# Kernel tuning notes

Measured on AMD Instinct MI355X. Metric: run time of the kernel, lower is better.

Reference implementation:

```python
import jax, jax.numpy as jnp
import numpy as np

VOCAB = 100000
EMB_DIM = 128
MAX_KP = 50  # config.max_num_keyphrases; lens tensors are constant-filled with this
EPS = 1e-8   # torch cosine_similarity eps


def setup_inputs() -> dict:
    key = jax.random.key(0)
    k1, k2, k3, k4 = jax.random.split(key, 4)
    B, A, K = 64, 32, 50
    batch_source = jax.random.randint(k1, (B, A, K), 0, VOCAB)
    pos_result = jax.random.randint(k2, (B, A, K), 0, VOCAB)
    neg_result = jax.random.randint(k3, (B, A, K), 0, VOCAB)
    emb_table = jax.random.normal(k4, (VOCAB + 1, EMB_DIM), dtype=jnp.float32)
    emb_table = emb_table.at[0].set(0.0)  # padding_idx=0
    return {
        "batch_source": batch_source,
        "pos_result": pos_result,
        "neg_result": neg_result,
        "emb_table": emb_table,
    }


def _embed(emb_table, idx):
    # idx: [B, A, K] -> mean-pooled [B, A, D]; denominator is the constant MAX_KP
    emb = emb_table[idx]                      # [B, A, K, D] gather (memory-bound)
    return jnp.sum(emb, axis=-2) / MAX_KP     # [B, A, D]


def _l2norm(x):
    n = jnp.sqrt(jnp.sum(x * x, axis=-1, keepdims=True))
    return x / jnp.maximum(n, EPS)


def _max_cosine(src_e, tgt_e):
    # src_e: [B, A1, D], tgt_e: [B, A2, D] -> max over all (A1, A2) pairs, per batch
    sims = jnp.einsum("bad,bcd->bac", _l2norm(src_e), _l2norm(tgt_e))  # [B, A1, A2]
    return jnp.max(sims, axis=(1, 2))  # [B]


def reference(batch_source, pos_result, neg_result, emb_table):
    src_e = _embed(emb_table, batch_source)
    pos_e = _embed(emb_table, pos_result)
    neg_e = _embed(emb_table, neg_result)
    pos_scores = _max_cosine(src_e, pos_e)  # [B]
    neg_scores = _max_cosine(src_e, neg_e)  # [B]
    x = pos_scores - neg_scores
    # BCEWithLogitsLoss with target = 1: mean(softplus(-x))
    loss = jnp.mean(jax.nn.softplus(-x))
    return loss
```

## Files before the change

kernel.cpp:

```cpp
#include <hip/hip_runtime.h>
#include <math.h>

#define BB 64
#define AA 32
#define KK 50
#define DD 128
#define MAX_KP 50
#define EPS_CS 1e-8f

__global__ void embed_norm_kernel(const int* __restrict__ src,
                                  const int* __restrict__ pos,
                                  const int* __restrict__ neg,
                                  const float* __restrict__ table,
                                  float* __restrict__ out )
{
    const int vec = blockIdx.x;
    const int t  = vec >> 11;
    const int ba = vec & 2047;

    const int* idx_base = (t == 0) ? src : (t == 1) ? pos : neg;
    idx_base += ba * KK;

    const int d = threadIdx.x;
    float acc = 0.f;
    #pragma unroll
    for (int k = 0; k < KK; ++k) {
        const int row = idx_base[k];
        acc += table[(long)row * DD + d];
    }
    acc *= (1.0f / MAX_KP);

    float sq = acc * acc;
    #pragma unroll
    for (int off = 32; off > 0; off >>= 1) sq += __shfl_down(sq, off, 64);

    __shared__ float partial[2];
    const int wave = threadIdx.x >> 6;
    if ((threadIdx.x & 63) == 0) partial[wave] = sq;
    __syncthreads();
    const float n2 = partial[0] + partial[1];
    const float nrm = sqrtf(n2);
    const float inv = 1.0f / fmaxf(nrm, EPS_CS);

    out[(long)vec * DD + d] = acc * inv;
}

__global__ void cosine_loss_kernel(const float* __restrict__ embs,
                                   float* __restrict__ per_batch )
{
    const int b = blockIdx.x;
    __shared__ float s_src[AA][DD + 1];
    __shared__ float s_pos[AA][DD + 1];
    __shared__ float s_neg[AA][DD + 1];

    const long base = (long)b * AA * DD;
    const float* src = embs + base;
    const float* pos = embs + (long)BB * AA * DD + base;
    const float* neg = embs + 2L * BB * AA * DD + base;

    const int tid = threadIdx.x;
    for (int i = tid; i < AA * DD; i += 256) {
        const int r = i >> 7, c = i & 127;
        s_src[r][c] = src[i];
        s_pos[r][c] = pos[i];
        s_neg[r][c] = neg[i];
    }
    __syncthreads();

    float pmax = -1e30f, nmax = -1e30f;
    #pragma unroll
    for (int p = 0; p < 4; ++p) {
        const int pair = tid + p * 256;
        const int i = pair >> 5;
        const int j = pair & 31;
        float dp = 0.f, dn = 0.f;
        #pragma unroll 8
        for (int d = 0; d < DD; ++d) {
            const float s = s_src[i][d];
            dp += s * s_pos[j][d];
            dn += s * s_neg[j][d];
        }
        pmax = fmaxf(pmax, dp);
        nmax = fmaxf(nmax, dn);
    }

    #pragma unroll
    for (int off = 32; off > 0; off >>= 1) {
        pmax = fmaxf(pmax, __shfl_down(pmax, off, 64));
        nmax = fmaxf(nmax, __shfl_down(nmax, off, 64));
    }
    __shared__ float sp[4], sn[4];
    const int wave = tid >> 6;
    if ((tid & 63) == 0) { sp[wave] = pmax; sn[wave] = nmax; }
    __syncthreads();

    if (tid == 0) {
        const float P = fmaxf(fmaxf(sp[0], sp[1]), fmaxf(sp[2], sp[3]));
        const float N = fmaxf(fmaxf(sn[0], sn[1]), fmaxf(sn[2], sn[3]));
        const float x = P - N;
        const float l = (x >= 0.f) ? log1pf(expf(-x)) : (-x + log1pf(expf(x)));
        per_batch[b] = l;
    }
}

__global__ void mean_kernel(const float* __restrict__ per_batch,
                            float* __restrict__ out)
{
    const int tid = threadIdx.x;
    float v = per_batch[tid];
    #pragma unroll
    for (int off = 32; off > 0; off >>= 1) v += __shfl_down(v, off, 64);
    if (tid == 0) out[0] = v * (1.0f / BB);
}

extern "C" void kernel_launch(void* const* d_in, const int* in_sizes, int n_in,
                              void* d_out, int out_size, void* d_ws, size_t ws_size,
                              hipStream_t stream) {
    const int*   batch_source = (const int*)d_in[0];
    const int*   pos_result   = (const int*)d_in[1];
    const int*   neg_result   = (const int*)d_in[2];
    const float* emb_table    = (const float*)d_in[3];
    float* out = (float*)d_out;

    float* embs      = (float*)d_ws;
    float* per_batch = embs + 3L * BB * AA * DD;

    embed_norm_kernel<<<3 * BB * AA, DD, 0, stream>>>(
        batch_source, pos_result, neg_result, emb_table, embs);
    cosine_loss_kernel<<<BB, 256, 0, stream>>>(embs, per_batch);
    mean_kernel<<<1, 64, 0, stream>>>(per_batch, out);
}
```

Baseline: 39.57 us.

## Vectorize embedding gather, register-tile cosine dots, fuse mean via atomic counter

The embedding kernel now assigns one 32-lane group per output vector and loads float4 rows. Indices are fetched once per lane and broadcast with shuffles, which removes the block-level shared-memory norm reduction. The cosine kernel loads shared memory with float4 and computes a 2x2 register tile of dot products per thread with float4 shared reads, cutting shared-memory traffic. The separate mean kernel is dropped: the last cosine block, found through an atomic counter, sums the per-batch losses, saving one launch at the cost of atomics and a serial 64-element sum.

```diff
diff --git a/kernel.cpp b/kernel.cpp
--- a/kernel.cpp
+++ b/kernel.cpp
@@ -7,87 +7,107 @@
 #define DD 128
 #define MAX_KP 50
 #define EPS_CS 1e-8f
+#define NVEC (3 * BB * AA)
+#define VPB 8
 
-__global__ void embed_norm_kernel(const int* __restrict__ src,
-                                  const int* __restrict__ pos,
-                                  const int* __restrict__ neg,
-                                  const float* __restrict__ table,
-                                  float* __restrict__ out )
-{
-    const int vec = blockIdx.x;
-    const int t  = vec >> 11;
-    const int ba = vec & 2047;
-
-    const int* idx_base = (t == 0) ? src : (t == 1) ? pos : neg;
-    idx_base += ba * KK;
-
-    const int d = threadIdx.x;
-    float acc = 0.f;
-    #pragma unroll
-    for (int k = 0; k < KK; ++k) {
-        const int row = idx_base[k];
-        acc += table[(long)row * DD + d];
-    }
-    acc *= (1.0f / MAX_KP);
-
-    float sq = acc * acc;
-    #pragma unroll
-    for (int off = 32; off > 0; off >>= 1) sq += __shfl_down(sq, off, 64);
-
-    __shared__ float partial[2];
-    const int wave = threadIdx.x >> 6;
-    if ((threadIdx.x & 63) == 0) partial[wave] = sq;
-    __syncthreads();
-    const float n2 = partial[0] + partial[1];
-    const float nrm = sqrtf(n2);
-    const float inv = 1.0f / fmaxf(nrm, EPS_CS);
-
-    out[(long)vec * DD + d] = acc * inv;
+__device__ __forceinline__ float dot4(float4 a, float4 b) {
+    return a.x * b.x + a.y * b.y + a.z * b.z + a.w * b.w;
 }
 
-__global__ void cosine_loss_kernel(const float* __restrict__ embs,
-                                   float* __restrict__ per_batch )
+__global__ __launch_bounds__(256) void embed_norm_kernel(
+    const int* __restrict__ src, const int* __restrict__ pos,
+    const int* __restrict__ neg, const float* __restrict__ table,
+    float* __restrict__ out, unsigned* __restrict__ counter)
 {
-    const int b = blockIdx.x;
-    __shared__ float s_src[AA][DD + 1];
-    __shared__ float s_pos[AA][DD + 1];
-    __shared__ float s_neg[AA][DD + 1];
+    if (blockIdx.x == 0 && threadIdx.x == 0) *counter = 0u;
 
-    const long base = (long)b * AA * DD;
-    const float* src = embs + base;
-    const float* pos = embs + (long)BB * AA * DD + base;
-    const float* neg = embs + 2L * BB * AA * DD + base;
+    const int tid  = threadIdx.x;
+    const int lane = tid & 31;
+    const int vec  = blockIdx.x * VPB + (tid >> 5);
+    const int t    = vec >> 11;
+    const int ba   = vec & 2047;
+    const int* idx = ((t == 0) ? src : (t == 1) ? pos : neg) + ba * KK;
 
+    int i0 = idx[lane];
+    int i1 = (lane < (KK - 32)) ? idx[32 + lane] : 0;
+
+    const float4* tab4 = (const float4*)table;
+    float4 acc = make_float4(0.f, 0.f, 0.f, 0.f);
+    #pragma unroll
+    for (int k = 0; k < 32; ++k) {
+        const int row = __shfl(i0, k, 32);
+        const float4 v = tab4[row * 32 + lane];
+        acc.x += v.x; acc.y += v.y; acc.z += v.z; acc.w += v.w;
+    }
+    #pragma unroll
+    for (int k = 0; k < KK - 32; ++k) {
+        const int row = __shfl(i1, k, 32);
+        const float4 v = tab4[row * 32 + lane];
+        acc.x += v.x; acc.y += v.y; acc.z += v.z; acc.w += v.w;
+    }
+
+    const float s = 1.0f / MAX_KP;
+    acc.x *= s; acc.y *= s; acc.z *= s; acc.w *= s;
+
+    float sq = dot4(acc, acc);
+    #pragma unroll
+    for (int off = 16; off > 0; off >>= 1) sq += __shfl_xor(sq, off, 32);
+
+    const float inv = 1.0f / fmaxf(sqrtf(sq), EPS_CS);
+    acc.x *= inv; acc.y *= inv; acc.z *= inv; acc.w *= inv;
+
+    ((float4*)out)[vec * 32 + lane] = acc;
+}
+
+__global__ __launch_bounds__(256) void cosine_loss_kernel(
+    const float* __restrict__ embs, float* __restrict__ per_batch,
+    unsigned* __restrict__ counter, float* __restrict__ out)
+{
+    const int b   = blockIdx.x;
     const int tid = threadIdx.x;
-    for (int i = tid; i < AA * DD; i += 256) {
-        const int r = i >> 7, c = i & 127;
-        s_src[r][c] = src[i];
-        s_pos[r][c] = pos[i];
-        s_neg[r][c] = neg[i];
+
+    __shared__ float s_src[AA][DD + 4];
+    __shared__ float s_pos[AA][DD + 4];
+    __shared__ float s_neg[AA][DD + 4];
+
+    const float4* src4 = (const float4*)(embs + (long)b * AA * DD);
+    const float4* pos4 = (const float4*)(embs + (long)(BB + b) * AA * DD);
+    const float4* neg4 = (const float4*)(embs + (long)(2 * BB + b) * AA * DD);
+
+    for (int i = tid; i < AA * DD / 4; i += 256) {
+        const int r = i >> 5, c = i & 31;
+        *(float4*)&s_src[r][c * 4] = src4[i];
+        *(float4*)&s_pos[r][c * 4] = pos4[i];
+        *(float4*)&s_neg[r][c * 4] = neg4[i];
     }
     __syncthreads();
 
-    float pmax = -1e30f, nmax = -1e30f;
-    #pragma unroll
-    for (int p = 0; p < 4; ++p) {
-        const int pair = tid + p * 256;
-        const int i = pair >> 5;
-        const int j = pair & 31;
-        float dp = 0.f, dn = 0.f;
-        #pragma unroll 8
-        for (int d = 0; d < DD; ++d) {
-            const float s = s_src[i][d];
-            dp += s * s_pos[j][d];
-            dn += s * s_neg[j][d];
-        }
-        pmax = fmaxf(pmax, dp);
-        nmax = fmaxf(nmax, dn);
+    const int ib = tid >> 4;
+    const int jb = tid & 15;
+
+    float dp00 = 0, dp01 = 0, dp10 = 0, dp11 = 0;
+    float dn00 = 0, dn01 = 0, dn10 = 0, dn11 = 0;
+    #pragma unroll 8
+    for (int d0 = 0; d0 < DD; d0 += 4) {
+        const float4 a0 = *(const float4*)&s_src[ib][d0];
+        const float4 a1 = *(const float4*)&s_src[ib + 16][d0];
+        const float4 p0 = *(const float4*)&s_pos[jb][d0];
+        const float4 p1 = *(const float4*)&s_pos[jb + 16][d0];
+        const float4 n0 = *(const float4*)&s_neg[jb][d0];
+        const float4 n1 = *(const float4*)&s_neg[jb + 16][d0];
+        dp00 += dot4(a0, p0); dp01 += dot4(a0, p1);
+        dp10 += dot4(a1, p0); dp11 += dot4(a1, p1);
+        dn00 += dot4(a0, n0); dn01 += dot4(a0, n1);
+        dn10 += dot4(a1, n0); dn11 += dot4(a1, n1);
     }
+
+    float pmax = fmaxf(fmaxf(dp00, dp01), fmaxf(dp10, dp11));
+    float nmax = fmaxf(fmaxf(dn00, dn01), fmaxf(dn10, dn11));
 
     #pragma unroll
     for (int off = 32; off > 0; off >>= 1) {
-        pmax = fmaxf(pmax, __shfl_down(pmax, off, 64));
-        nmax = fmaxf(nmax, __shfl_down(nmax, off, 64));
+        pmax = fmaxf(pmax, __shfl_xor(pmax, off, 64));
+        nmax = fmaxf(nmax, __shfl_xor(nmax, off, 64));
     }
     __shared__ float sp[4], sn[4];
     const int wave = tid >> 6;
@@ -99,18 +119,21 @@
         const float N = fmaxf(fmaxf(sn[0], sn[1]), fmaxf(sn[2], sn[3]));
         const float x = P - N;
         const float l = (x >= 0.f) ? log1pf(expf(-x)) : (-x + log1pf(expf(x)));
-        per_batch[b] = l;
+
+        __hip_atomic_store(&per_batch[b], l, __ATOMIC_RELEASE,
+                           __HIP_MEMORY_SCOPE_AGENT);
+        const unsigned old = __hip_atomic_fetch_add(
+            counter, 1u, __ATOMIC_ACQ_REL, __HIP_MEMORY_SCOPE_AGENT);
+        if (old == BB - 1) {
+            float acc = 0.f;
+            for (int i = 0; i < BB; ++i)
+                acc += __hip_atomic_load(&per_batch[i], __ATOMIC_ACQUIRE,
+                                         __HIP_MEMORY_SCOPE_AGENT);
+            out[0] = acc * (1.0f / BB);
+            __hip_atomic_store(counter, 0u, __ATOMIC_RELAXED,
+                               __HIP_MEMORY_SCOPE_AGENT);
+        }
     }
-}
-
-__global__ void mean_kernel(const float* __restrict__ per_batch,
-                            float* __restrict__ out)
-{
-    const int tid = threadIdx.x;
-    float v = per_batch[tid];
-    #pragma unroll
-    for (int off = 32; off > 0; off >>= 1) v += __shfl_down(v, off, 64);
-    if (tid == 0) out[0] = v * (1.0f / BB);
 }
 
 extern "C" void kernel_launch(void* const* d_in, const int* in_sizes, int n_in,
@@ -122,11 +145,11 @@
     const float* emb_table    = (const float*)d_in[3];
     float* out = (float*)d_out;
 
-    float* embs      = (float*)d_ws;
-    float* per_batch = embs + 3L * BB * AA * DD;
+    float*    embs      = (float*)d_ws;
+    float*    per_batch = embs + 3L * BB * AA * DD;
+    unsigned* counter   = (unsigned*)(per_batch + BB);
 
-    embed_norm_kernel<<<3 * BB * AA, DD, 0, stream>>>(
-        batch_source, pos_result, neg_result, emb_table, embs);
-    cosine_loss_kernel<<<BB, 256, 0, stream>>>(embs, per_batch);
-    mean_kernel<<<1, 64, 0, stream>>>(per_batch, out);
+    embed_norm_kernel<<<NVEC / VPB, 256, 0, stream>>>(
+        batch_source, pos_result, neg_result, emb_table, embs, counter);
+    cosine_loss_kernel<<<BB, 256, 0, stream>>>(embs, per_batch, counter, out);
 }
```

Measured after the change: 46.31 us. 17.0% more time.

## Split cosine stage across more blocks and vectorize embedding gather

Applied to the files above, without the earlier changes.

The embedding kernel now has each wave gather a different half of the keyphrase rows with float2 loads, then merges the two partial sums through shared memory before normalizing. The cosine kernel is split into four blocks per batch (pos/neg × src half) using float4 shared-memory dot products, so 256 blocks run instead of 64. A finalize kernel combines the partial maxima and computes the mean softplus loss. The aim is better latency hiding in the gather and more occupancy in the cosine stage, at the cost of an extra partial buffer and one shared-memory merge per vector.

```diff
diff --git a/kernel.cpp b/kernel.cpp
--- a/kernel.cpp
+++ b/kernel.cpp
@@ -7,110 +7,115 @@
 #define DD 128
 #define MAX_KP 50
 #define EPS_CS 1e-8f
+#define NVEC (3 * BB * AA)
 
-__global__ void embed_norm_kernel(const int* __restrict__ src,
-                                  const int* __restrict__ pos,
-                                  const int* __restrict__ neg,
-                                  const float* __restrict__ table,
-                                  float* __restrict__ out )
+__device__ __forceinline__ float dot4(float4 a, float4 b) {
+    return a.x * b.x + a.y * b.y + a.z * b.z + a.w * b.w;
+}
+
+__global__ __launch_bounds__(128) void embed_norm_kernel(
+    const int* __restrict__ src, const int* __restrict__ pos,
+    const int* __restrict__ neg, const float* __restrict__ table,
+    float* __restrict__ out)
 {
     const int vec = blockIdx.x;
-    const int t  = vec >> 11;
-    const int ba = vec & 2047;
+    const int t   = vec >> 11;
+    const int ba  = vec & 2047;
+    const int* idx = ((t == 0) ? src : (t == 1) ? pos : neg) + ba * KK;
 
-    const int* idx_base = (t == 0) ? src : (t == 1) ? pos : neg;
-    idx_base += ba * KK;
+    const int l = threadIdx.x & 63;
+    const int w = __builtin_amdgcn_readfirstlane(threadIdx.x >> 6);
 
-    const int d = threadIdx.x;
-    float acc = 0.f;
+    const float2* tab2 = (const float2*)table;
+    float2 acc = make_float2(0.f, 0.f);
     #pragma unroll
-    for (int k = 0; k < KK; ++k) {
-        const int row = idx_base[k];
-        acc += table[(long)row * DD + d];
+    for (int i = 0; i < KK / 2; ++i) {
+        const int row = idx[2 * i + w];
+        const float2 v = tab2[(long)row * 64 + l];
+        acc.x += v.x; acc.y += v.y;
     }
-    acc *= (1.0f / MAX_KP);
 
-    float sq = acc * acc;
-    #pragma unroll
-    for (int off = 32; off > 0; off >>= 1) sq += __shfl_down(sq, off, 64);
+    __shared__ float2 s_part[64];
+    if (threadIdx.x >= 64) s_part[l] = acc;
+    __syncthreads();
 
-    __shared__ float partial[2];
-    const int wave = threadIdx.x >> 6;
-    if ((threadIdx.x & 63) == 0) partial[wave] = sq;
-    __syncthreads();
-    const float n2 = partial[0] + partial[1];
-    const float nrm = sqrtf(n2);
-    const float inv = 1.0f / fmaxf(nrm, EPS_CS);
+    if (threadIdx.x < 64) {
+        const float2 p = s_part[l];
+        acc.x = (acc.x + p.x) * (1.0f / MAX_KP);
+        acc.y = (acc.y + p.y) * (1.0f / MAX_KP);
 
-    out[(long)vec * DD + d] = acc * inv;
+        float sq = acc.x * acc.x + acc.y * acc.y;
+        #pragma unroll
+        for (int off = 32; off > 0; off >>= 1) sq += __shfl_xor(sq, off, 64);
+
+        const float inv = 1.0f / fmaxf(sqrtf(sq), EPS_CS);
+        acc.x *= inv; acc.y *= inv;
+
+        ((float2*)out)[(long)vec * 64 + l] = acc;
+    }
 }
 
-__global__ void cosine_loss_kernel(const float* __restrict__ embs,
-                                   float* __restrict__ per_batch )
+__global__ __launch_bounds__(256) void cosine_part_kernel(
+    const float* __restrict__ embs, float* __restrict__ part )
 {
-    const int b = blockIdx.x;
-    __shared__ float s_src[AA][DD + 1];
-    __shared__ float s_pos[AA][DD + 1];
-    __shared__ float s_neg[AA][DD + 1];
+    const int blk = blockIdx.x;
+    const int b   = blk >> 2;
+    const int q   = blk & 3;
+    const int tens  = q >> 1;
+    const int ihalf = q & 1;
+    const int tid = threadIdx.x;
 
-    const long base = (long)b * AA * DD;
-    const float* src = embs + base;
-    const float* pos = embs + (long)BB * AA * DD + base;
-    const float* neg = embs + 2L * BB * AA * DD + base;
+    __shared__ float s_src[16][DD + 4];
+    __shared__ float s_tgt[AA][DD + 4];
 
-    const int tid = threadIdx.x;
-    for (int i = tid; i < AA * DD; i += 256) {
-        const int r = i >> 7, c = i & 127;
-        s_src[r][c] = src[i];
-        s_pos[r][c] = pos[i];
-        s_neg[r][c] = neg[i];
+    const float4* src4 = (const float4*)(embs + ((long)b * AA + ihalf * 16) * DD);
+    const float4* tgt4 = (const float4*)(embs + (long)(BB + tens * BB + b) * AA * DD);
+
+    for (int i = tid; i < 16 * DD / 4; i += 256) {
+        const int r = i >> 5, c = i & 31;
+        *(float4*)&s_src[r][c * 4] = src4[i];
+    }
+    for (int i = tid; i < AA * DD / 4; i += 256) {
+        const int r = i >> 5, c = i & 31;
+        *(float4*)&s_tgt[r][c * 4] = tgt4[i];
     }
     __syncthreads();
 
-    float pmax = -1e30f, nmax = -1e30f;
-    #pragma unroll
-    for (int p = 0; p < 4; ++p) {
-        const int pair = tid + p * 256;
-        const int i = pair >> 5;
-        const int j = pair & 31;
-        float dp = 0.f, dn = 0.f;
-        #pragma unroll 8
-        for (int d = 0; d < DD; ++d) {
-            const float s = s_src[i][d];
-            dp += s * s_pos[j][d];
-            dn += s * s_neg[j][d];
-        }
-        pmax = fmaxf(pmax, dp);
-        nmax = fmaxf(nmax, dn);
+    const int si = tid >> 4;
+    const int j  = tid & 15;
+
+    float d0s = 0.f, d1s = 0.f;
+    #pragma unroll 8
+    for (int d0 = 0; d0 < DD; d0 += 4) {
+        const float4 a  = *(const float4*)&s_src[si][d0];
+        const float4 t0 = *(const float4*)&s_tgt[j][d0];
+        const float4 t1 = *(const float4*)&s_tgt[j + 16][d0];
+        d0s += dot4(a, t0);
+        d1s += dot4(a, t1);
     }
+    float m = fmaxf(d0s, d1s);
 
     #pragma unroll
-    for (int off = 32; off > 0; off >>= 1) {
-        pmax = fmaxf(pmax, __shfl_down(pmax, off, 64));
-        nmax = fmaxf(nmax, __shfl_down(nmax, off, 64));
-    }
-    __shared__ float sp[4], sn[4];
-    const int wave = tid >> 6;
-    if ((tid & 63) == 0) { sp[wave] = pmax; sn[wave] = nmax; }
+    for (int off = 32; off > 0; off >>= 1) m = fmaxf(m, __shfl_xor(m, off, 64));
+    __shared__ float sm[4];
+    if ((tid & 63) == 0) sm[tid >> 6] = m;
     __syncthreads();
 
-    if (tid == 0) {
-        const float P = fmaxf(fmaxf(sp[0], sp[1]), fmaxf(sp[2], sp[3]));
-        const float N = fmaxf(fmaxf(sn[0], sn[1]), fmaxf(sn[2], sn[3]));
-        const float x = P - N;
-        const float l = (x >= 0.f) ? log1pf(expf(-x)) : (-x + log1pf(expf(x)));
-        per_batch[b] = l;
-    }
+    if (tid == 0)
+        part[blk] = fmaxf(fmaxf(sm[0], sm[1]), fmaxf(sm[2], sm[3]));
 }
 
-__global__ void mean_kernel(const float* __restrict__ per_batch,
-                            float* __restrict__ out)
+__global__ void finalize_kernel(const float* __restrict__ part,
+                                float* __restrict__ out)
 {
-    const int tid = threadIdx.x;
-    float v = per_batch[tid];
+    const int b = threadIdx.x;
+    const float P = fmaxf(part[b * 4 + 0], part[b * 4 + 1]);
+    const float N = fmaxf(part[b * 4 + 2], part[b * 4 + 3]);
+    const float x = P - N;
+    float l = (x >= 0.f) ? log1pf(expf(-x)) : (-x + log1pf(expf(x)));
     #pragma unroll
-    for (int off = 32; off > 0; off >>= 1) v += __shfl_down(v, off, 64);
-    if (tid == 0) out[0] = v * (1.0f / BB);
+    for (int off = 32; off > 0; off >>= 1) l += __shfl_xor(l, off, 64);
+    if (b == 0) out[0] = l * (1.0f / BB);
 }
 
 extern "C" void kernel_launch(void* const* d_in, const int* in_sizes, int n_in,
@@ -122,11 +127,11 @@
     const float* emb_table    = (const float*)d_in[3];
     float* out = (float*)d_out;
 
-    float* embs      = (float*)d_ws;
-    float* per_batch = embs + 3L * BB * AA * DD;
+    float* embs = (float*)d_ws;
+    float* part = embs + 3L * BB * AA * DD;
 
-    embed_norm_kernel<<<3 * BB * AA, DD, 0, stream>>>(
+    embed_norm_kernel<<<NVEC, 128, 0, stream>>>(
         batch_source, pos_result, neg_result, emb_table, embs);
-    cosine_loss_kernel<<<BB, 256, 0, stream>>>(embs, per_batch);
-    mean_kernel<<<1, 64, 0, stream>>>(per_batch, out);
+    cosine_part_kernel<<<4 * BB, 256, 0, stream>>>(embs, part);
+    finalize_kernel<<<1, 64, 0, stream>>>(part, out);
 }
```

Measured after the change: 34.51 us. -12.8%, faster.
